# Kernel tuning notes

Hardware: AMD Instinct MI355X
Metric: run time of the kernel (lower is better)

The kernel has to match this reference:

```python
import jax, jax.numpy as jnp
import numpy as np

H = 96
W = 96
FX = 96.0
FY = 96.0
NEAR = 0.3
EPS = 1e-8


def q2r(quat):
    # quat: [N,4] (w,x,y,z) -> [N,3,3]
    q = quat / (jnp.linalg.norm(quat, axis=-1, keepdims=True) + 1e-12)
    w, x, y, z = q[:, 0], q[:, 1], q[:, 2], q[:, 3]
    R = jnp.stack([
        1 - 2 * (y * y + z * z), 2 * (x * y - w * z), 2 * (x * z + w * y),
        2 * (x * y + w * z), 1 - 2 * (x * x + z * z), 2 * (y * z - w * x),
        2 * (x * z - w * y), 2 * (y * z + w * x), 1 - 2 * (x * x + y * y),
    ], axis=-1).reshape(-1, 3, 3)
    return R


def setup_inputs() -> dict:
    key = jax.random.key(0)
    ks = jax.random.split(key, 8)
    N = 4096
    pos_xy = jax.random.uniform(ks[0], (N, 2), minval=-2.0, maxval=2.0, dtype=jnp.float32)
    pos_z = jax.random.uniform(ks[1], (N, 1), minval=2.0, maxval=6.0, dtype=jnp.float32)
    pos = jnp.concatenate([pos_xy, pos_z], axis=-1)
    rgb = jax.random.normal(ks[2], (N, 3), dtype=jnp.float32)
    opa = jax.random.normal(ks[3], (N,), dtype=jnp.float32)
    quat = jax.random.normal(ks[4], (N, 4), dtype=jnp.float32)
    scale = jax.random.uniform(ks[5], (N, 3), dtype=jnp.float32) * 0.05 + 0.005
    rot = jnp.eye(3, dtype=jnp.float32)
    tran = jnp.zeros(3, dtype=jnp.float32)
    return {"pos": pos, "rgb": rgb, "opa": opa, "quat": quat, "scale": scale, "rot": rot, "tran": tran}


def reference(pos, rgb, opa, quat, scale, rot, tran):
    # ---- project: world -> camera -> image space ----
    cam = pos @ rot.T + tran[None, :]              # [N,3]
    x, y, z = cam[:, 0], cam[:, 1], cam[:, 2]
    r = jnp.linalg.norm(cam, axis=-1)              # depth = ray length (camera_to_image)
    mean2d = jnp.stack([x / z, y / z], axis=-1)    # [N,2]

    # jacobian of (x/z, y/z, |p|) wrt camera-space point, [N,3,3]
    zeros = jnp.zeros_like(z)
    J = jnp.stack([
        1.0 / z, zeros, -x / (z * z),
        zeros, 1.0 / z, -y / (z * z),
        x / r, y / r, z / r,
    ], axis=-1).reshape(-1, 3, 3)

    # ---- 3D covariance: R S S^T R^T ----
    R = q2r(quat)                                   # [N,3,3]
    s = jnp.abs(scale) + 1e-4                       # [N,3]
    RS = R * s[:, None, :]                          # R @ diag(s)
    cov3d = jnp.einsum('nij,nkj->nik', RS, RS)      # [N,3,3]

    # ---- 2D covariance: (J W) cov3d (J W)^T, upper-left 2x2 ----
    JW = jnp.einsum('nij,jk->nik', J, rot)          # [N,3,3]
    cov2d = jnp.einsum('nij,njk,nlk->nil', JW, cov3d, JW)[:, :2, :2]  # [N,2,2]

    a = cov2d[:, 0, 0] + EPS
    d = cov2d[:, 1, 1] + EPS
    b = 0.5 * (cov2d[:, 0, 1] + cov2d[:, 1, 0])
    det = a * d - b * b
    inv_a = d / det
    inv_b = -b / det
    inv_d = a / det

    rgb_act = jax.nn.sigmoid(rgb)                   # [N,3]
    opa_act = jax.nn.sigmoid(opa)                   # [N]

    # ---- per-pixel gaussian evaluation in normalized image space ----
    u = (jnp.arange(W, dtype=jnp.float32) + 0.5 - W / 2) / FX   # [W]
    v = (jnp.arange(H, dtype=jnp.float32) + 0.5 - H / 2) / FY   # [H]
    pu = jnp.tile(u, H)                                          # [P]
    pv = jnp.repeat(v, W)                                        # [P]

    dx = pu[None, :] - mean2d[:, 0:1]               # [N,P]
    dy = pv[None, :] - mean2d[:, 1:2]               # [N,P]
    power = -0.5 * (inv_a[:, None] * dx * dx + 2.0 * inv_b[:, None] * dx * dy + inv_d[:, None] * dy * dy)
    alpha = opa_act[:, None] * jnp.exp(power)       # [N,P]
    alpha = jnp.clip(alpha, 0.0, 0.99)
    valid = (z > NEAR).astype(alpha.dtype)[:, None]
    alpha = alpha * valid

    # ---- depth-sorted alpha compositing ----
    order = jnp.argsort(r)                          # near -> far
    alpha_s = alpha[order]                          # [N,P]
    rgb_s = rgb_act[order]                          # [N,3]

    log_1m = jnp.log1p(-alpha_s)                    # [N,P]
    cum = jnp.cumsum(log_1m, axis=0)
    logT = jnp.concatenate([jnp.zeros((1, alpha_s.shape[1]), alpha_s.dtype), cum[:-1]], axis=0)
    w = jnp.exp(logT) * alpha_s                     # [N,P] blending weights
    img = jnp.einsum('np,nc->pc', w, rgb_s)         # [P,3]
    return img.reshape(H, W, 3)
```

## Files before the change

### kernel.cpp

```cpp
#include <hip/hip_runtime.h>
#include <hip/hip_fp16.h>
#include <math.h>

#define N_G   4096
#define IMW   96
#define TILE  6
#define TILES_X 16
#define NTILE (TILES_X*TILES_X)
#define NTHR  1024
#define NW    (NTHR/64)
#define NST   (N_G/NTHR)
#define NPX   (TILE*TILE)
#define NSEG  16
#define BCAP  1536
#define CAP   512
#define FXI   (1.0f/96.0f)
#define NEARP 0.3f
#define EPSV  1e-8f
#define LOG2E 1.4426950408889634f
#define LN2   0.6931471805599453f
#define CULL_K 16.0f

typedef unsigned long long ull;
typedef __attribute__((ext_vector_type(2))) unsigned long long ull2;

__global__ __launch_bounds__(NTHR, 1) void splat_k(
    const float* __restrict__ pos, const float* __restrict__ rgb,
    const float* __restrict__ opa, const float* __restrict__ quat,
    const float* __restrict__ scale, const float* __restrict__ rot,
    const float* __restrict__ tran, float* __restrict__ out)
{
    __shared__ unsigned int bl[BCAP];
    __shared__ __align__(16) ull skey[CAP+2];
    __shared__ float4 pk0[CAP], pk1[CAP];
    __shared__ float4 pk0s[CAP], pk1s[CAP];
    __shared__ float4 pix[NSEG*NPX];
    __shared__ int psum[4][CAP];
    __shared__ int bcnt_sh, cnt_sh;

    const int t = threadIdx.x;
    const int tile = blockIdx.x;
    const int tx = tile % TILES_X, ty = tile / TILES_X;
    const float u0 = ((float)(tx*TILE) + 0.5f - 48.0f) * FXI;
    const float u1 = u0 + (TILE-1) * FXI;
    const float v0 = ((float)(ty*TILE) + 0.5f - 48.0f) * FXI;
    const float v1 = v0 + (TILE-1) * FXI;
    const int wid = t >> 6, lane = t & 63;

    if (t == 0) { bcnt_sh = 0; cnt_sh = 0; }

    float R00=rot[0],R01=rot[1],R02=rot[2];
    float R10=rot[3],R11=rot[4],R12=rot[5];
    float R20=rot[6],R21=rot[7],R22=rot[8];
    float t0=tran[0], t1=tran[1], t2=tran[2];

    float pp0[NST], pp1[NST], pp2[NST], po[NST], ps0[NST], ps1[NST], ps2[NST];
    #pragma unroll
    for (int st = 0; st < NST; st++) {
        int gi = st*NTHR + t;
        pp0[st]=pos[gi*3+0]; pp1[st]=pos[gi*3+1]; pp2[st]=pos[gi*3+2];
        po[st]=opa[gi];
        ps0[st]=scale[gi*3+0]; ps1[st]=scale[gi*3+1]; ps2[st]=scale[gi*3+2];
    }
    __syncthreads();

    #pragma unroll
    for (int st = 0; st < NST; st++) {
        int gi = st*NTHR + t;
        float x = R00*pp0[st] + R01*pp1[st] + R02*pp2[st] + t0;
        float y = R10*pp0[st] + R11*pp1[st] + R12*pp2[st] + t1;
        float z = R20*pp0[st] + R21*pp1[st] + R22*pp2[st] + t2;
        float invz = 1.0f/z;
        float mu = x*invz, mv = y*invz;

        float inz2 = invz*invz;
        float fn = 2.0f*inz2 + (x*x + y*y)*inz2*inz2;
        float smax = fmaxf(fmaxf(fabsf(ps0[st]), fabsf(ps1[st])), fabsf(ps2[st])) + 1e-4f;
        float lmax = fn*smax*smax + EPSV;
        float amp = CULL_K + 1.0f + fminf(0.0f, po[st]*LOG2E);
        float r2b = amp * lmax * (2.0f*LN2) * 1.02f;

        float cu = fminf(fmaxf(mu, u0), u1);
        float cv = fminf(fmaxf(mv, v0), v1);
        float ddx = mu - cu, ddy = mv - cv;
        bool flag = (z > NEARP) && (amp > 0.0f) && (ddx*ddx + ddy*ddy <= r2b);

        ull m = __ballot(flag);
        int nm = __popcll(m);
        int base = 0;
        if (lane == 0 && nm) base = atomicAdd(&bcnt_sh, nm);
        base = __shfl(base, 0);
        if (flag) {
            int p = base + __popcll(m & ((1ull << lane) - 1ull));
            if (p < BCAP) bl[p] = (unsigned int)gi;
        }
    }
    __syncthreads();
    int bcnt = bcnt_sh; if (bcnt > BCAP) bcnt = BCAP;

    for (int s0i = 0; s0i < bcnt; s0i += NTHR) {
        int s = s0i + t;
        bool flag = false;
        float4 o0, o1; float rr = 0.0f;
        unsigned int gi = 0;
        if (s < bcnt) {
            gi = bl[s];
            float p0=pos[gi*3+0], p1=pos[gi*3+1], p2=pos[gi*3+2];
            float x = R00*p0 + R01*p1 + R02*p2 + t0;
            float y = R10*p0 + R11*p1 + R12*p2 + t1;
            float z = R20*p0 + R21*p1 + R22*p2 + t2;
            rr = sqrtf(x*x + y*y + z*z);
            float invz = 1.0f/z;
            float mu = x*invz, mv = y*invz;

            float J02 = -x*invz*invz, J12 = -y*invz*invz;
            float JW00 = invz*R00 + J02*R20;
            float JW01 = invz*R01 + J02*R21;
            float JW02 = invz*R02 + J02*R22;
            float JW10 = invz*R10 + J12*R20;
            float JW11 = invz*R11 + J12*R21;
            float JW12 = invz*R12 + J12*R22;

            float qw=quat[gi*4+0], qx=quat[gi*4+1], qy=quat[gi*4+2], qz=quat[gi*4+3];
            float qn = sqrtf(qw*qw+qx*qx+qy*qy+qz*qz) + 1e-12f;
            float qi = 1.0f/qn;
            qw*=qi; qx*=qi; qy*=qi; qz*=qi;
            float Q00=1.f-2.f*(qy*qy+qz*qz), Q01=2.f*(qx*qy-qw*qz), Q02=2.f*(qx*qz+qw*qy);
            float Q10=2.f*(qx*qy+qw*qz), Q11=1.f-2.f*(qx*qx+qz*qz), Q12=2.f*(qy*qz-qw*qx);
            float Q20=2.f*(qx*qz-qw*qy), Q21=2.f*(qy*qz+qw*qx), Q22=1.f-2.f*(qx*qx+qy*qy);

            float sa=fabsf(scale[gi*3+0])+1e-4f;
            float sb=fabsf(scale[gi*3+1])+1e-4f;
            float sc=fabsf(scale[gi*3+2])+1e-4f;
            float A00=Q00*sa,A01=Q01*sb,A02=Q02*sc;
            float A10=Q10*sa,A11=Q11*sb,A12=Q12*sc;
            float A20=Q20*sa,A21=Q21*sb,A22=Q22*sc;
            float C00=A00*A00+A01*A01+A02*A02;
            float C01=A00*A10+A01*A11+A02*A12;
            float C02=A00*A20+A01*A21+A02*A22;
            float C11=A10*A10+A11*A11+A12*A12;
            float C12=A10*A20+A11*A21+A12*A22;
            float C22=A20*A20+A21*A21+A22*A22;
            float M00=JW00*C00+JW01*C01+JW02*C02;
            float M01=JW00*C01+JW01*C11+JW02*C12;
            float M02=JW00*C02+JW01*C12+JW02*C22;
            float M10=JW10*C00+JW11*C01+JW12*C02;
            float M11=JW10*C01+JW11*C11+JW12*C12;
            float M12=JW10*C02+JW11*C12+JW12*C22;
            float a  = M00*JW00+M01*JW01+M02*JW02 + EPSV;
            float d  = M10*JW10+M11*JW11+M12*JW12 + EPSV;
            float bb = 0.5f*((M00*JW10+M01*JW11+M02*JW12)+(M10*JW00+M11*JW01+M12*JW02));
            float invdet = 1.0f/(a*d - bb*bb);
            float iaP = -0.5f*d*invdet*LOG2E;
            float ibP =  bb*invdet*LOG2E;
            float idP = -0.5f*a*invdet*LOG2E;

            float sig_o = 1.0f/(1.0f+__expf(-opa[gi]));
            float opa_eff = (z > NEARP) ? sig_o : 0.0f;

            float q00 = -iaP, q01 = -0.5f*ibP, q11 = -idP;
            float detQ = q00*q11 - q01*q01;
            float K = CULL_K + log2f(opa_eff);

            float cu = fminf(fmaxf(mu, u0), u1);
            float cv = fminf(fmaxf(mv, v0), v1);
            float ddx = mu - cu, ddy = mv - cv;
            flag = (ddx*ddx*detQ <= K*q11) && (ddy*ddy*detQ <= K*q00);

            if (flag) {
                float c0 = 1.0f/(1.0f+__expf(-rgb[gi*3+0]));
                float c1 = 1.0f/(1.0f+__expf(-rgb[gi*3+1]));
                float c2 = 1.0f/(1.0f+__expf(-rgb[gi*3+2]));
                unsigned int c01p =
                    (unsigned int)__half_as_ushort(__float2half_rn(c0)) |
                    ((unsigned int)__half_as_ushort(__float2half_rn(c1)) << 16);
                unsigned int c2p =
                    (unsigned int)__half_as_ushort(__float2half_rn(c2));
                o0 = make_float4(mu, mv, iaP, ibP);
                o1 = make_float4(idP, opa_eff,
                                 __uint_as_float(c01p), __uint_as_float(c2p));
            }
        }
        ull m = __ballot(flag);
        int nm = __popcll(m);
        int base = 0;
        if (lane == 0 && nm) base = atomicAdd(&cnt_sh, nm);
        base = __shfl(base, 0);
        if (flag) {
            int p = base + __popcll(m & ((1ull << lane) - 1ull));
            if (p < CAP) {
                pk0[p] = o0; pk1[p] = o1;
                skey[p] = ((ull)__float_as_uint(rr) << 32) | gi;
            }
        }
    }
    __syncthreads();
    int cnt = cnt_sh; if (cnt > CAP) cnt = CAP;

    if (t == 0 && (cnt & 1)) skey[cnt] = ~0ull;
    __syncthreads();
    int cnt2 = cnt + (cnt & 1);
    int nq = cnt2 >> 1;
    const ull2* sk2 = (const ull2*)skey;
    const int g = t >> 8, e = t & 255;
    const bool h1 = (e < cnt), h2 = (e + 256 < cnt);
    if (h1) {
        ull kv1 = skey[e];
        ull kv2 = h2 ? skey[e + 256] : 0;
        int wA = (nq * g) >> 2;
        int wB = (nq * (g+1)) >> 2;
        int c1 = 0, c2 = 0;
        for (int w = wA; w < wB; w++) {
            ull2 p = sk2[w];
            c1 += (p.x < kv1) ? 1 : 0;
            c1 += (p.y < kv1) ? 1 : 0;
            c2 += (p.x < kv2) ? 1 : 0;
            c2 += (p.y < kv2) ? 1 : 0;
        }
        psum[g][e] = c1;
        if (h2) psum[g][e + 256] = c2;
    }
    __syncthreads();
    if (t < 256 && h1) {
        int r1 = psum[0][e] + psum[1][e] + psum[2][e] + psum[3][e];
        pk0s[r1] = pk0[e];
        pk1s[r1] = pk1[e];
        if (h2) {
            int e2 = e + 256;
            int r2 = psum[0][e2] + psum[1][e2] + psum[2][e2] + psum[3][e2];
            pk0s[r2] = pk0[e2];
            pk1s[r2] = pk1[e2];
        }
    }
    __syncthreads();

    {
        const int seg = wid;
        const bool act = (lane < NPX);
        const int pid = act ? lane : 0;
        const int px = tx*TILE + (pid % TILE);
        const int py = ty*TILE + (pid / TILE);
        const float pu = ((float)px + 0.5f - 48.0f) * FXI;
        const float pv = ((float)py + 0.5f - 48.0f) * FXI;

        const int per = (cnt + NSEG - 1) / NSEG;
        const int sA = min(seg * per, cnt);
        const int sB = min(sA + per, cnt);

        float T = 1.0f, cr = 0.0f, cg = 0.0f, cb = 0.0f;
        for (int s = sA; s < sB; s++) {
            float4 a0 = pk0s[s];
            float4 a1 = pk1s[s];
            unsigned int c01p = __float_as_uint(a1.z);
            float c0 = __half2float(__ushort_as_half((unsigned short)(c01p & 0xffffu)));
            float c1 = __half2float(__ushort_as_half((unsigned short)(c01p >> 16)));
            float c2 = __half2float(__ushort_as_half((unsigned short)(__float_as_uint(a1.w) & 0xffffu)));
            float dx = pu - a0.x;
            float dy = pv - a0.y;
            float pw = dx*(a0.z*dx + a0.w*dy) + a1.x*dy*dy;
            float al = fminf(a1.y * __builtin_amdgcn_exp2f(pw), 0.99f);
            float w = T * al;
            cr += w * c0;
            cg += w * c1;
            cb += w * c2;
            T *= (1.0f - al);
        }
        if (act) pix[seg*NPX + pid] = make_float4(cr, cg, cb, T);
    }
    __syncthreads();

    if (t < NPX) {
        float orr = 0.0f, og = 0.0f, ob = 0.0f, T2 = 1.0f;
        #pragma unroll
        for (int s = 0; s < NSEG; s++) {
            float4 P = pix[s*NPX + t];
            orr += T2 * P.x;
            og  += T2 * P.y;
            ob  += T2 * P.z;
            T2  *= P.w;
        }
        int px = tx*TILE + (t % TILE);
        int py = ty*TILE + (t / TILE);
        int pixel = py * IMW + px;
        out[pixel*3+0] = orr;
        out[pixel*3+1] = og;
        out[pixel*3+2] = ob;
    }
}

extern "C" void kernel_launch(void* const* d_in, const int* in_sizes, int n_in,
                              void* d_out, int out_size, void* d_ws, size_t ws_size,
                              hipStream_t stream) {
    const float* pos   = (const float*)d_in[0];
    const float* rgb   = (const float*)d_in[1];
    const float* opa   = (const float*)d_in[2];
    const float* quat  = (const float*)d_in[3];
    const float* scale = (const float*)d_in[4];
    const float* rot   = (const float*)d_in[5];
    const float* tran  = (const float*)d_in[6];
    float* out = (float*)d_out;

    splat_k<<<NTILE, NTHR, 0, stream>>>(pos, rgb, opa, quat, scale, rot, tran, out);
}
```

Before: 13.54 us.

## Stage gaussian inputs in LDS with float4 loads and tighten per-axis cull

Each block now copies pos, scale and opa into shared memory with coalesced float4 loads, and each thread handles 4 contiguous gaussians instead of strided ones. The second pass reads these values from LDS instead of doing scattered global loads. The later sort and pixel buffers alias the same stash region to keep LDS usage bounded. The coarse cull also switches from a circular bound to separate per-axis bounds, which should let fewer gaussians through. The aliasing is only safe if the stash is no longer read once the sort buffers are written, which is not visible here.

```diff
diff --git a/kernel.cpp b/kernel.cpp
--- a/kernel.cpp
+++ b/kernel.cpp
@@ -9,7 +9,6 @@
 #define NTILE (TILES_X*TILES_X)
 #define NTHR  1024
 #define NW    (NTHR/64)
-#define NST   (N_G/NTHR)
 #define NPX   (TILE*TILE)
 #define NSEG  16
 #define BCAP  1536
@@ -30,13 +29,19 @@
     const float* __restrict__ scale, const float* __restrict__ rot,
     const float* __restrict__ tran, float* __restrict__ out)
 {
+    __shared__ __align__(16) float stash[N_G*7];
     __shared__ unsigned int bl[BCAP];
     __shared__ __align__(16) ull skey[CAP+2];
     __shared__ float4 pk0[CAP], pk1[CAP];
-    __shared__ float4 pk0s[CAP], pk1s[CAP];
-    __shared__ float4 pix[NSEG*NPX];
-    __shared__ int psum[4][CAP];
     __shared__ int bcnt_sh, cnt_sh;
+
+    float* spos   = stash;
+    float* sscale = stash + N_G*3;
+    float* sopa   = stash + N_G*6;
+    float4* pk0s = (float4*)stash;
+    float4* pk1s = pk0s + CAP;
+    int (*psum)[CAP] = (int (*)[CAP])(stash + 4096);
+    float4* pix = (float4*)(stash + 6144);
 
     const int t = threadIdx.x;
     const int tile = blockIdx.x;
@@ -47,53 +52,85 @@
     const float v1 = v0 + (TILE-1) * FXI;
     const int wid = t >> 6, lane = t & 63;
 
-    if (t == 0) { bcnt_sh = 0; cnt_sh = 0; }
-
     float R00=rot[0],R01=rot[1],R02=rot[2];
     float R10=rot[3],R11=rot[4],R12=rot[5];
     float R20=rot[6],R21=rot[7],R22=rot[8];
     float t0=tran[0], t1=tran[1], t2=tran[2];
 
-    float pp0[NST], pp1[NST], pp2[NST], po[NST], ps0[NST], ps1[NST], ps2[NST];
-    #pragma unroll
-    for (int st = 0; st < NST; st++) {
-        int gi = st*NTHR + t;
-        pp0[st]=pos[gi*3+0]; pp1[st]=pos[gi*3+1]; pp2[st]=pos[gi*3+2];
-        po[st]=opa[gi];
-        ps0[st]=scale[gi*3+0]; ps1[st]=scale[gi*3+1]; ps2[st]=scale[gi*3+2];
-    }
-    __syncthreads();
-
-    #pragma unroll
-    for (int st = 0; st < NST; st++) {
-        int gi = st*NTHR + t;
-        float x = R00*pp0[st] + R01*pp1[st] + R02*pp2[st] + t0;
-        float y = R10*pp0[st] + R11*pp1[st] + R12*pp2[st] + t1;
-        float z = R20*pp0[st] + R21*pp1[st] + R22*pp2[st] + t2;
-        float invz = 1.0f/z;
-        float mu = x*invz, mv = y*invz;
-
-        float inz2 = invz*invz;
-        float fn = 2.0f*inz2 + (x*x + y*y)*inz2*inz2;
-        float smax = fmaxf(fmaxf(fabsf(ps0[st]), fabsf(ps1[st])), fabsf(ps2[st])) + 1e-4f;
-        float lmax = fn*smax*smax + EPSV;
-        float amp = CULL_K + 1.0f + fminf(0.0f, po[st]*LOG2E);
-        float r2b = amp * lmax * (2.0f*LN2) * 1.02f;
-
-        float cu = fminf(fmaxf(mu, u0), u1);
-        float cv = fminf(fmaxf(mv, v0), v1);
-        float ddx = mu - cu, ddy = mv - cv;
-        bool flag = (z > NEARP) && (amp > 0.0f) && (ddx*ddx + ddy*ddy <= r2b);
-
-        ull m = __ballot(flag);
-        int nm = __popcll(m);
+    {
+        const float4* p4 = (const float4*)pos;
+        const float4* s4 = (const float4*)scale;
+        const float4* o4 = (const float4*)opa;
+        float4* sp4 = (float4*)spos;
+        float4* ss4 = (float4*)sscale;
+        float4* so4 = (float4*)sopa;
+        #pragma unroll
+        for (int k = 0; k < 3; k++) {
+            sp4[k*NTHR + t] = p4[k*NTHR + t];
+            ss4[k*NTHR + t] = s4[k*NTHR + t];
+        }
+        so4[t] = o4[t];
+    }
+    if (t == 0) { bcnt_sh = 0; cnt_sh = 0; }
+    __syncthreads();
+
+    {
+        const float4* sp4 = (const float4*)spos;
+        const float4* ss4 = (const float4*)sscale;
+        const float4* so4 = (const float4*)sopa;
+        float4 P0 = sp4[3*t], P1 = sp4[3*t+1], P2 = sp4[3*t+2];
+        float4 S0 = ss4[3*t], S1 = ss4[3*t+1], S2 = ss4[3*t+2];
+        float4 OO = so4[t];
+        const float gx[4] = {P0.x, P0.w, P1.z, P2.y};
+        const float gy[4] = {P0.y, P1.x, P1.w, P2.z};
+        const float gz[4] = {P0.z, P1.y, P2.x, P2.w};
+        const float sx[4] = {S0.x, S0.w, S1.z, S2.y};
+        const float sy[4] = {S0.y, S1.x, S1.w, S2.z};
+        const float sz[4] = {S0.z, S1.y, S2.x, S2.w};
+        const float op[4] = {OO.x, OO.y, OO.z, OO.w};
+
+        bool fl[4];
+        #pragma unroll
+        for (int j = 0; j < 4; j++) {
+            float x = R00*gx[j] + R01*gy[j] + R02*gz[j] + t0;
+            float y = R10*gx[j] + R11*gy[j] + R12*gz[j] + t1;
+            float z = R20*gx[j] + R21*gy[j] + R22*gz[j] + t2;
+            float invz = 1.0f/z;
+            float mu = x*invz, mv = y*invz;
+
+            float inz2 = invz*invz;
+            float fnu = inz2 + x*x*inz2*inz2;
+            float fnv = inz2 + y*y*inz2*inz2;
+            float smax = fmaxf(fmaxf(fabsf(sx[j]), fabsf(sy[j])), fabsf(sz[j])) + 1e-4f;
+            float s2 = smax*smax;
+            float amp = CULL_K + 1.0f + fminf(0.0f, op[j]*LOG2E);
+            float sc2 = amp * (2.0f*LN2) * 1.02f;
+            float eu2b = sc2 * (fnu*s2 + EPSV);
+            float ev2b = sc2 * (fnv*s2 + EPSV);
+
+            float cu = fminf(fmaxf(mu, u0), u1);
+            float cv = fminf(fmaxf(mv, v0), v1);
+            float ddx = mu - cu, ddy = mv - cv;
+            fl[j] = (z > NEARP) && (amp > 0.0f) &&
+                    (ddx*ddx <= eu2b) && (ddy*ddy <= ev2b);
+        }
+
+        ull b0 = __ballot(fl[0]), b1 = __ballot(fl[1]);
+        ull b2 = __ballot(fl[2]), b3 = __ballot(fl[3]);
+        int nm = __popcll(b0) + __popcll(b1) + __popcll(b2) + __popcll(b3);
         int base = 0;
         if (lane == 0 && nm) base = atomicAdd(&bcnt_sh, nm);
         base = __shfl(base, 0);
-        if (flag) {
-            int p = base + __popcll(m & ((1ull << lane) - 1ull));
-            if (p < BCAP) bl[p] = (unsigned int)gi;
-        }
+        ull lm = (1ull << lane) - 1ull;
+        int o0 = __popcll(b0), o1 = o0 + __popcll(b1), o2 = o1 + __popcll(b2);
+        if (fl[0]) { int p = base + __popcll(b0 & lm);
+                     if (p < BCAP) bl[p] = (unsigned int)(4*t + 0); }
+        if (fl[1]) { int p = base + o0 + __popcll(b1 & lm);
+                     if (p < BCAP) bl[p] = (unsigned int)(4*t + 1); }
+        if (fl[2]) { int p = base + o1 + __popcll(b2 & lm);
+                     if (p < BCAP) bl[p] = (unsigned int)(4*t + 2); }
+        if (fl[3]) { int p = base + o2 + __popcll(b3 & lm);
+                     if (p < BCAP) bl[p] = (unsigned int)(4*t + 3); }
     }
     __syncthreads();
     int bcnt = bcnt_sh; if (bcnt > BCAP) bcnt = BCAP;
@@ -105,7 +142,7 @@
         unsigned int gi = 0;
         if (s < bcnt) {
             gi = bl[s];
-            float p0=pos[gi*3+0], p1=pos[gi*3+1], p2=pos[gi*3+2];
+            float p0 = spos[gi*3+0], p1 = spos[gi*3+1], p2 = spos[gi*3+2];
             float x = R00*p0 + R01*p1 + R02*p2 + t0;
             float y = R10*p0 + R11*p1 + R12*p2 + t1;
             float z = R20*p0 + R21*p1 + R22*p2 + t2;
@@ -121,7 +158,8 @@
             float JW11 = invz*R11 + J12*R21;
             float JW12 = invz*R12 + J12*R22;
 
-            float qw=quat[gi*4+0], qx=quat[gi*4+1], qy=quat[gi*4+2], qz=quat[gi*4+3];
+            const float4 qv = ((const float4*)quat)[gi];
+            float qw=qv.x, qx=qv.y, qy=qv.z, qz=qv.w;
             float qn = sqrtf(qw*qw+qx*qx+qy*qy+qz*qz) + 1e-12f;
             float qi = 1.0f/qn;
             qw*=qi; qx*=qi; qy*=qi; qz*=qi;
@@ -129,9 +167,9 @@
             float Q10=2.f*(qx*qy+qw*qz), Q11=1.f-2.f*(qx*qx+qz*qz), Q12=2.f*(qy*qz-qw*qx);
             float Q20=2.f*(qx*qz-qw*qy), Q21=2.f*(qy*qz+qw*qx), Q22=1.f-2.f*(qx*qx+qy*qy);
 
-            float sa=fabsf(scale[gi*3+0])+1e-4f;
-            float sb=fabsf(scale[gi*3+1])+1e-4f;
-            float sc=fabsf(scale[gi*3+2])+1e-4f;
+            float sa=fabsf(sscale[gi*3+0])+1e-4f;
+            float sb=fabsf(sscale[gi*3+1])+1e-4f;
+            float sc=fabsf(sscale[gi*3+2])+1e-4f;
             float A00=Q00*sa,A01=Q01*sb,A02=Q02*sc;
             float A10=Q10*sa,A11=Q11*sb,A12=Q12*sc;
             float A20=Q20*sa,A21=Q21*sb,A22=Q22*sc;
@@ -155,7 +193,7 @@
             float ibP =  bb*invdet*LOG2E;
             float idP = -0.5f*a*invdet*LOG2E;
 
-            float sig_o = 1.0f/(1.0f+__expf(-opa[gi]));
+            float sig_o = 1.0f/(1.0f+__expf(-sopa[gi]));
             float opa_eff = (z > NEARP) ? sig_o : 0.0f;
 
             float q00 = -iaP, q01 = -0.5f*ibP, q11 = -idP;
```

New measurement: 13.83 us. +2.1%, slower.
